# Optimization experiments

Measured on AMD Instinct MI355X. Metric: run time of the kernel, lower is better.

Reference implementation:

```python
import jax, jax.numpy as jnp
import numpy as np

N, E = 50000, 800000
H, C, K = 8, 16, 4
LAMBD = 1.0
DECAY = [float(np.log(LAMBD / (k + 1) + (1 + 1e-06))) for k in range(K + 1)]


def setup_inputs() -> dict:
    key = jax.random.key(0)
    ks = jax.random.split(key, 10)
    s = 0.05  # keep activations stable over K hops
    return {
        "x": jax.random.normal(ks[0], (N, 256), jnp.float32),
        "edge_index": jax.random.randint(ks[1], (2, E), 0, N, jnp.int64),
        "W0": jax.random.normal(ks[2], (256, 128), jnp.float32) * s,
        "b0": jnp.zeros((128,), jnp.float32),
        "W1": jax.random.normal(ks[3], (128, 128), jnp.float32) * s,
        "b1": jnp.zeros((128,), jnp.float32),
        "Wout": jax.random.normal(ks[4], (128, 40), jnp.float32) * s,
        "bout": jnp.zeros((40,), jnp.float32),
        "hop_att0": jax.random.normal(ks[5], (H, C), jnp.float32) * s,
        "hop_atts": jax.random.normal(ks[6], (K, H, 2 * C), jnp.float32) * s,
        "atts": jax.random.normal(ks[7], (K, H, C), jnp.float32) * s,
        "hop_biases": jnp.ones((K + 1, H), jnp.float32),
    }


def _aero_forward(x, edge_index, W0, b0, W1, b1, Wout, bout,
                  hop_att0, hop_atts, atts, hop_biases):
    n = x.shape[0]
    # add self loops (cached_edge_index is None in the torch module)
    loops = jnp.arange(n, dtype=edge_index.dtype)
    row = jnp.concatenate([edge_index[0], loops])  # source j
    col = jnp.concatenate([edge_index[1], loops])  # target i

    # hid_feat_init (dropout p=0 -> identity); num_layers=2
    h = x @ W0 + b0
    h = jax.nn.elu(h) @ W1 + b1
    h = h.reshape(n, H, C)

    # k = 0 hop attention
    g = jnp.einsum('hc,nhc->nh', hop_att0, jax.nn.elu(h)) + hop_biases[0]
    z = h * g[..., None]
    z_scale = z * DECAY[0]

    for k in range(1, K + 1):
        # edge attention: gather, elementwise, degree-normalize
        zi = z_scale[col]          # [E', H, C] target
        zj = z_scale[row]          # [E', H, C] source
        a = jnp.einsum('hc,ehc->eh', atts[k - 1], jax.nn.elu(zi + zj))
        a = jax.nn.softplus(a) + 1e-06                       # [E', H]
        deg = jax.ops.segment_sum(a, col, num_segments=n)    # [N, H]
        dinv = jnp.where(deg > 0, deg ** -0.5, 0.0)
        a = dinv[row] * a * dinv[col]
        # propagate: scatter-add weighted source features onto targets
        h = jax.ops.segment_sum(a[..., None] * h[row], col, num_segments=n)
        # hop attention on concat(h, z_scale)
        hz = jax.nn.elu(jnp.concatenate([h, z_scale], axis=-1))  # [N, H, 2C]
        g = jnp.einsum('hc,nhc->nh', hop_atts[k - 1], hz) + hop_biases[k]
        z = z + h * g[..., None]
        z_scale = z * DECAY[k]

    # node classifier
    z = jax.nn.elu(z.reshape(n, H * C))
    return z @ Wout + bout


def reference(x, edge_index, W0, b0, W1, b1, Wout, bout,
              hop_att0, hop_atts, atts, hop_biases):
    return _aero_forward(x, edge_index, W0, b0, W1, b1, Wout, bout,
                         hop_att0, hop_atts, atts, hop_biases)
```

## Files before the change

### kernel.cpp

```cpp
#include <hip/hip_runtime.h>
#include <hip/hip_fp16.h>
#include <math.h>

#define NH 8
#define NC 16
#define HC 128

typedef __attribute__((ext_vector_type(4))) _Float16 half4;
typedef __attribute__((ext_vector_type(8))) _Float16 half8;

__device__ __forceinline__ float eluf(float x) { return x > 0.f ? x : __expf(x) - 1.f; }
__device__ __forceinline__ float splusf(float x) { return fmaxf(x, 0.f) + __logf(1.f + __expf(-fabsf(x))); }

#if __has_builtin(__builtin_amdgcn_exp2f)
#define EXP2F(x) __builtin_amdgcn_exp2f(x)
#else
#define EXP2F(x) exp2f(x)
#endif

__global__ void count_kernel(const int* __restrict__ ei, int* __restrict__ cnt, int E, int E2) {
    int e = blockIdx.x * blockDim.x + threadIdx.x;
    if (e >= E2) return;
    int col = (e < E) ? ei[E + e] : (e - E);
    atomicAdd(&cnt[col], 1);
}

__global__ void scan1_kernel(const int* __restrict__ counts, int* __restrict__ ptr,
                             int* __restrict__ partials, int n) {
    __shared__ int tmp[256];
    int t = threadIdx.x;
    int i = blockIdx.x * 256 + t;
    int v = (i < n) ? counts[i] : 0;
    tmp[t] = v;
    __syncthreads();
    for (int off = 1; off < 256; off <<= 1) {
        int add = (t >= off) ? tmp[t - off] : 0;
        __syncthreads();
        tmp[t] += add;
        __syncthreads();
    }
    if (i < n) ptr[i] = tmp[t] - v;
    if (t == 255) partials[blockIdx.x] = tmp[255];
}

__global__ void scan2_kernel(int* __restrict__ partials, int nb) {
    __shared__ int tmp[256];
    int t = threadIdx.x;
    int v = (t < nb) ? partials[t] : 0;
    tmp[t] = v;
    __syncthreads();
    for (int off = 1; off < 256; off <<= 1) {
        int add = (t >= off) ? tmp[t - off] : 0;
        __syncthreads();
        tmp[t] += add;
        __syncthreads();
    }
    if (t < nb) partials[t] = tmp[t] - v;
}

__global__ void scan3_kernel(int* __restrict__ ptr, const int* __restrict__ partials,
                             int n, int total) {
    int i = blockIdx.x * 256 + threadIdx.x;
    if (i < n) ptr[i] += partials[blockIdx.x];
    if (i == 0) ptr[n] = total;
}

__global__ void fill_kernel(const int* __restrict__ ei, const int* __restrict__ ptr,
                            int* __restrict__ cursor, int* __restrict__ src, int E, int E2) {
    int e = blockIdx.x * blockDim.x + threadIdx.x;
    if (e >= E2) return;
    int col, row;
    if (e < E) { row = ei[e]; col = ei[E + e]; }
    else       { row = e - E; col = e - E; }
    int pos = ptr[col] + atomicAdd(&cursor[col], 1);
    src[pos] = row;
}

template<int K, bool ELU_OUT, bool HOP0>
__global__ __launch_bounds__(256)
void mlp_gemm(const float* __restrict__ A, const float* __restrict__ W,
              const float* __restrict__ bias, float* __restrict__ out, int M,
              float* __restrict__ z_out, _Float16* __restrict__ h16_out,
              _Float16* __restrict__ z16_out,
              const float* __restrict__ att0, const float* __restrict__ hb0) {
    __shared__ float As[16 * 68];
    __shared__ float Ws[16 * 132];
    const int tid = threadIdx.x;
    const int m0 = blockIdx.x * 64;
    const int tm = tid >> 4;
    const int tn = tid & 15;
    float acc[4][8];
#pragma unroll
    for (int i = 0; i < 4; ++i)
#pragma unroll
        for (int j = 0; j < 8; ++j) acc[i][j] = 0.f;

    const int ra = tid >> 2;
    const int qa = (tid & 3) * 4;

    for (int k0 = 0; k0 < K; k0 += 16) {
        float4 a = make_float4(0.f, 0.f, 0.f, 0.f);
        int garow = m0 + ra;
        if (garow < M) a = *(const float4*)(A + (size_t)garow * K + k0 + qa);
        float wv[8];
#pragma unroll
        for (int t = 0; t < 8; ++t) {
            int idx = tid + t * 256;
            int r = idx >> 7, c = idx & 127;
            wv[t] = W[(size_t)(k0 + r) * 128 + c];
        }
        __syncthreads();
        As[(qa + 0) * 68 + ra] = a.x; As[(qa + 1) * 68 + ra] = a.y;
        As[(qa + 2) * 68 + ra] = a.z; As[(qa + 3) * 68 + ra] = a.w;
#pragma unroll
        for (int t = 0; t < 8; ++t) {
            int idx = tid + t * 256;
            int r = idx >> 7, c = idx & 127;
            Ws[r * 132 + c] = wv[t];
        }
        __syncthreads();
#pragma unroll
        for (int kk = 0; kk < 16; ++kk) {
            float ar[4], wr[8];
            *(float4*)&ar[0] = *(const float4*)&As[kk * 68 + tm * 4];
            *(float4*)&wr[0] = *(const float4*)&Ws[kk * 132 + tn * 4];
            *(float4*)&wr[4] = *(const float4*)&Ws[kk * 132 + 64 + tn * 4];
#pragma unroll
            for (int i = 0; i < 4; ++i)
#pragma unroll
                for (int j = 0; j < 8; ++j)
                    acc[i][j] = fmaf(ar[i], wr[j], acc[i][j]);
        }
    }
#pragma unroll
    for (int i = 0; i < 4; ++i) {
        int r = m0 + tm * 4 + i;
        float vv[8];
#pragma unroll
        for (int c = 0; c < 2; ++c)
#pragma unroll
            for (int j = 0; j < 4; ++j) {
                float v = acc[i][c * 4 + j] + bias[c * 64 + tn * 4 + j];
                if (ELU_OUT) v = eluf(v);
                vv[c * 4 + j] = v;
            }
        if (HOP0) {
            float part[2];
#pragma unroll
            for (int c = 0; c < 2; ++c) {
                float p = 0.f;
#pragma unroll
                for (int j = 0; j < 4; ++j)
                    p += att0[c * 64 + tn * 4 + j] * eluf(vv[c * 4 + j]);
                p += __shfl_xor(p, 1);
                p += __shfl_xor(p, 2);
                part[c] = p;
            }
            if (r < M) {
#pragma unroll
                for (int c = 0; c < 2; ++c) {
                    float g = part[c] + hb0[4 * c + (tn >> 2)];
                    int coff = c * 64 + tn * 4;
                    _Float16* hp  = h16_out + ((size_t)r << 7) + coff;
                    _Float16* zhp = z16_out + ((size_t)r << 7) + coff;
                    float*    zp  = z_out   + ((size_t)r << 7) + coff;
                    half4 ho, zo;
                    float zz[4];
#pragma unroll
                    for (int j = 0; j < 4; ++j) zz[j] = vv[c * 4 + j] * g;
                    ho.x = (_Float16)vv[c * 4 + 0]; ho.y = (_Float16)vv[c * 4 + 1];
                    ho.z = (_Float16)vv[c * 4 + 2]; ho.w = (_Float16)vv[c * 4 + 3];
                    zo.x = (_Float16)zz[0]; zo.y = (_Float16)zz[1];
                    zo.z = (_Float16)zz[2]; zo.w = (_Float16)zz[3];
                    *(half4*)hp = ho;
                    *(half4*)zhp = zo;
                    *(float4*)zp = make_float4(zz[0], zz[1], zz[2], zz[3]);
                }
            }
        } else {
            if (r < M) {
#pragma unroll
                for (int c = 0; c < 2; ++c) {
                    float* op = out + (size_t)r * 128 + c * 64 + tn * 4;
                    *(float4*)op = make_float4(vv[c * 4 + 0], vv[c * 4 + 1],
                                               vv[c * 4 + 2], vv[c * 4 + 3]);
                }
            }
        }
    }
}

__global__ __launch_bounds__(256)
void passA_kernel(const _Float16* __restrict__ z16, const int* __restrict__ ptr,
                  const int* __restrict__ src, const float* __restrict__ att,
                  float decay, _Float16* __restrict__ a_e, float* __restrict__ dinv, int n) {
    int wid = (int)((blockIdx.x * 256u + threadIdx.x) >> 6);
    if (wid >= n) return;
    const int lane = threadIdx.x & 63;
    const int g  = lane >> 4;
    const int q  = lane & 15;
    const int hd = q >> 1;
    const unsigned i = (unsigned)wid;
    const float dl2 = decay * 1.44269504089f;

    float ziL[8];
    {
        const half8 zi = *(const half8*)(z16 + ((size_t)i << 7) + (q << 3));
#pragma unroll
        for (int c = 0; c < 8; ++c) ziL[c] = (float)zi[c] * dl2;
    }
    float av[8];
    *(float4*)&av[0] = *(const float4*)(att + (q << 3));
    *(float4*)&av[4] = *(const float4*)(att + (q << 3) + 4);
    float sav = ((av[0] + av[1]) + (av[2] + av[3]))
              + ((av[4] + av[5]) + (av[6] + av[7]));
    sav += __shfl_xor(sav, 1);

    const int s0 = ptr[wid], s1 = ptr[wid + 1];
    float dacc = 0.f;

#define PA_BODY(f, sv) do {                                                  \
        float pm = 0.f, pe = 0.f;                                            \
        _Pragma("unroll")                                                    \
        for (int c = 0; c < 8; ++c) {                                        \
            float y = fmaf((float)(f)[c], dl2, ziL[c]);                      \
            float e2 = EXP2F(fminf(y, 0.f));                                 \
            pm = fmaf(av[c], fmaxf(y, 0.f), pm);                             \
            pe = fmaf(av[c], e2, pe);                                        \
        }                                                                    \
        float pc = fmaf(pm, 0.69314718056f, pe);                             \
        pc += __shfl_xor(pc, 1);                                             \
        if ((q & 1) == 0) {                                                  \
            float aval = splusf(pc - sav) + 1e-6f;                           \
            a_e[((size_t)(sv) << 3) + hd] = (_Float16)aval;                  \
            dacc += aval;                                                    \
        }                                                                    \
    } while (0)

    const int nfull = (s1 - s0) & ~7;
    const int send = s0 + nfull;
    for (int s = s0 + g; s < send; s += 8) {
        unsigned ja = (unsigned)src[s];
        unsigned jb = (unsigned)src[s + 4];
        const half8 fa = *(const half8*)(z16 + ((size_t)ja << 7) + (q << 3));
        const half8 fb = *(const half8*)(z16 + ((size_t)jb << 7) + (q << 3));
        PA_BODY(fa, s);
        PA_BODY(fb, s + 4);
    }
    {
        int sA = send + g;
        if (sA < s1) {
            unsigned ja = (unsigned)src[sA];
            const half8 fa = *(const half8*)(z16 + ((size_t)ja << 7) + (q << 3));
            PA_BODY(fa, sA);
        }
        int sB = send + 4 + g;
        if (sB < s1) {
            unsigned jb = (unsigned)src[sB];
            const half8 fb = *(const half8*)(z16 + ((size_t)jb << 7) + (q << 3));
            PA_BODY(fb, sB);
        }
    }
#undef PA_BODY

    dacc += __shfl_xor(dacc, 16);
    dacc += __shfl_xor(dacc, 32);
    if ((lane & 0x31) == 0) {
        dinv[((size_t)i << 3) + hd] = (dacc > 0.f) ? (1.f / sqrtf(dacc)) : 0.f;
    }
}

__global__ __launch_bounds__(256)
void passB_kernel(const _Float16* __restrict__ h_in, float* __restrict__ z,
                  _Float16* __restrict__ z16,
                  const int* __restrict__ ptr, const int* __restrict__ src,
                  const _Float16* __restrict__ a_e, const float* __restrict__ dinv,
                  const float* __restrict__ hatt, const float* __restrict__ hb,
                  float decay, _Float16* __restrict__ h_out, int n, int store_h) {
    int wid = (int)((blockIdx.x * 256u + threadIdx.x) >> 6);
    if (wid >= n) return;
    const int lane = threadIdx.x & 63;
    const int g  = lane >> 4;
    const int q  = lane & 15;
    const int hd = q >> 1;
    const unsigned i = (unsigned)wid;

    const float di = dinv[((size_t)i << 3) + hd];
    const int s0 = ptr[wid], s1 = ptr[wid + 1];
    float acc[8];
#pragma unroll
    for (int c = 0; c < 8; ++c) acc[c] = 0.f;

    const int nfull = (s1 - s0) & ~7;
    const int send = s0 + nfull;
    for (int s = s0 + g; s < send; s += 8) {
        unsigned ja = (unsigned)src[s];
        unsigned jb = (unsigned)src[s + 4];
        const _Float16 aA = a_e[((size_t)s << 3) + hd];
        const _Float16 aB = a_e[((size_t)(s + 4) << 3) + hd];
        const float dA = dinv[((size_t)ja << 3) + hd];
        const float dB = dinv[((size_t)jb << 3) + hd];
        const half8 fa = *(const half8*)(h_in + ((size_t)ja << 7) + (q << 3));
        const half8 fb = *(const half8*)(h_in + ((size_t)jb << 7) + (q << 3));
        const float wa = (float)aA * dA;
        const float wb = (float)aB * dB;
#pragma unroll
        for (int c = 0; c < 8; ++c) acc[c] = fmaf((float)fa[c], wa, acc[c]);
#pragma unroll
        for (int c = 0; c < 8; ++c) acc[c] = fmaf((float)fb[c], wb, acc[c]);
    }
    {
        int sA = send + g;
        if (sA < s1) {
            unsigned j = (unsigned)src[sA];
            const float w = (float)a_e[((size_t)sA << 3) + hd] * dinv[((size_t)j << 3) + hd];
            const half8 f = *(const half8*)(h_in + ((size_t)j << 7) + (q << 3));
#pragma unroll
            for (int c = 0; c < 8; ++c) acc[c] = fmaf((float)f[c], w, acc[c]);
        }
        int sB = send + 4 + g;
        if (sB < s1) {
            unsigned j = (unsigned)src[sB];
            const float w = (float)a_e[((size_t)sB << 3) + hd] * dinv[((size_t)j << 3) + hd];
            const half8 f = *(const half8*)(h_in + ((size_t)j << 7) + (q << 3));
#pragma unroll
            for (int c = 0; c < 8; ++c) acc[c] = fmaf((float)f[c], w, acc[c]);
        }
    }
#pragma unroll
    for (int c = 0; c < 8; ++c) {
        acc[c] += __shfl_xor(acc[c], 16);
        acc[c] += __shfl_xor(acc[c], 32);
    }

    float hn[8];
#pragma unroll
    for (int c = 0; c < 8; ++c) hn[c] = di * acc[c];

    float* zrow = z + ((size_t)i << 7) + (q << 3);
    const float4 zva = *(const float4*)zrow;
    const float4 zvb = *(const float4*)(zrow + 4);
    float zv[8] = {zva.x, zva.y, zva.z, zva.w, zvb.x, zvb.y, zvb.z, zvb.w};

    const float* hA = hatt + hd * 32 + (q & 1) * 8;
    float p = 0.f;
#pragma unroll
    for (int c = 0; c < 8; ++c) p = fmaf(hA[c], eluf(hn[c]), p);
#pragma unroll
    for (int c = 0; c < 8; ++c) p = fmaf(hA[16 + c], eluf(zv[c] * decay), p);
    p += __shfl_xor(p, 1);
    const float gv = p + hb[hd];

    if (g == 0) {
        float zn[8];
#pragma unroll
        for (int c = 0; c < 8; ++c) zn[c] = fmaf(hn[c], gv, zv[c]);
        *(float4*)zrow       = make_float4(zn[0], zn[1], zn[2], zn[3]);
        *(float4*)(zrow + 4) = make_float4(zn[4], zn[5], zn[6], zn[7]);
        if (store_h) {
            half8 ho, zo;
#pragma unroll
            for (int c = 0; c < 8; ++c) { ho[c] = (_Float16)hn[c]; zo[c] = (_Float16)zn[c]; }
            *(half8*)(h_out + ((size_t)i << 7) + (q << 3)) = ho;
            *(half8*)(z16   + ((size_t)i << 7) + (q << 3)) = zo;
        }
    }
}

__global__ __launch_bounds__(256)
void gout_kernel(const float* __restrict__ z, const float* __restrict__ W,
                 const float* __restrict__ bias, float* __restrict__ out, int M) {
    __shared__ float zs[128 * 65];
    __shared__ float ws[128 * 40];
    const int tid = threadIdx.x;
    const int r0 = blockIdx.x * 64;
    for (int idx = tid; idx < 128 * 40; idx += 256) ws[idx] = W[idx];
    const int r = tid >> 2;
    const int q = tid & 3;
    {
        int grow = r0 + r;
#pragma unroll
        for (int t = 0; t < 8; ++t) {
            int k = q * 4 + t * 16;
            float4 v = make_float4(0.f, 0.f, 0.f, 0.f);
            if (grow < M) v = *(const float4*)(z + (size_t)grow * HC + k);
            zs[(k + 0) * 65 + r] = eluf(v.x);
            zs[(k + 1) * 65 + r] = eluf(v.y);
            zs[(k + 2) * 65 + r] = eluf(v.z);
            zs[(k + 3) * 65 + r] = eluf(v.w);
        }
    }
    __syncthreads();
    float acc[10];
#pragma unroll
    for (int j = 0; j < 10; ++j) acc[j] = bias[q * 10 + j];
    for (int k = 0; k < 128; ++k) {
        float zk = zs[k * 65 + r];
#pragma unroll
        for (int j = 0; j < 10; ++j)
            acc[j] = fmaf(zk, ws[k * 40 + q * 10 + j], acc[j]);
    }
    int grow = r0 + r;
    if (grow < M) {
        float* op = out + (size_t)grow * 40 + q * 10;
#pragma unroll
        for (int j = 0; j < 10; ++j) op[j] = acc[j];
    }
}

extern "C" void kernel_launch(void* const* d_in, const int* in_sizes, int n_in,
                              void* d_out, int out_size, void* d_ws, size_t ws_size,
                              hipStream_t stream) {
    (void)n_in; (void)out_size; (void)ws_size;
    const float* x    = (const float*)d_in[0];
    const int*   ei   = (const int*)d_in[1];
    const float* W0   = (const float*)d_in[2];
    const float* b0   = (const float*)d_in[3];
    const float* W1   = (const float*)d_in[4];
    const float* b1   = (const float*)d_in[5];
    const float* Wout = (const float*)d_in[6];
    const float* bout = (const float*)d_in[7];
    const float* att0 = (const float*)d_in[8];
    const float* hatts= (const float*)d_in[9];
    const float* atts = (const float*)d_in[10];
    const float* hb   = (const float*)d_in[11];
    float* out = (float*)d_out;

    const int N  = in_sizes[0] / 256;
    const int E  = in_sizes[1] / 2;
    const int E2 = E + N;

    char* p = (char*)d_ws;
    auto carve = [&](size_t bytes) -> char* {
        char* r = p;
        p += (bytes + 255) & ~(size_t)255;
        return r;
    };
    float*    h1     = (float*)carve((size_t)N * HC * 4);
    _Float16* hbufA  = (_Float16*)carve((size_t)N * HC * 2);
    _Float16* hbufB  = (_Float16*)carve((size_t)N * HC * 2);
    float*    zbuf   = (float*)carve((size_t)N * HC * 4);
    _Float16* z16buf = (_Float16*)carve((size_t)N * HC * 2);
    _Float16* a_e    = (_Float16*)carve((size_t)E2 * NH * 2);
    float*    dinvb  = (float*)carve((size_t)N * NH * 4);
    int* csr_ptr   = (int*)carve((size_t)(N + 1) * 4);
    int* csr_src   = (int*)carve((size_t)E2 * 4);
    int* cursor    = (int*)carve((size_t)N * 4);
    int* partials  = (int*)carve(1024 * 4);

    float decay[5];
    for (int k = 0; k <= 4; ++k) decay[k] = (float)log(1.0 / (k + 1) + 1.0 + 1e-6);

    hipMemsetAsync(cursor, 0, (size_t)N * 4, stream);
    int eb = (E2 + 255) / 256;
    int nb = (N + 255) / 256;
    count_kernel<<<eb, 256, 0, stream>>>(ei, cursor, E, E2);
    scan1_kernel<<<nb, 256, 0, stream>>>(cursor, csr_ptr, partials, N);
    scan2_kernel<<<1, 256, 0, stream>>>(partials, nb);
    scan3_kernel<<<nb, 256, 0, stream>>>(csr_ptr, partials, N, E2);
    hipMemsetAsync(cursor, 0, (size_t)N * 4, stream);
    fill_kernel<<<eb, 256, 0, stream>>>(ei, csr_ptr, cursor, csr_src, E, E2);

    int gb = (N + 63) / 64;
    mlp_gemm<256, true , false><<<gb, 256, 0, stream>>>(x,  W0, b0, h1, N,
                                                        nullptr, nullptr, nullptr,
                                                        nullptr, nullptr);
    mlp_gemm<128, false, true ><<<gb, 256, 0, stream>>>(h1, W1, b1, nullptr, N,
                                                        zbuf, hbufA, z16buf, att0, hb);

    _Float16* hin  = hbufA;
    _Float16* hout = hbufB;
    int wb = (N + 3) / 4;
    for (int k = 1; k <= 4; ++k) {
        passA_kernel<<<wb, 256, 0, stream>>>(z16buf, csr_ptr, csr_src,
                                             atts + (size_t)(k - 1) * NH * NC,
                                             decay[k - 1], a_e, dinvb, N);
        passB_kernel<<<wb, 256, 0, stream>>>(hin, zbuf, z16buf, csr_ptr, csr_src,
                                             a_e, dinvb,
                                             hatts + (size_t)(k - 1) * NH * 32,
                                             hb + (size_t)k * NH, decay[k - 1], hout, N,
                                             (k < 4) ? 1 : 0);
        _Float16* t = hin; hin = hout; hout = t;
    }

    gout_kernel<<<(N + 63) / 64, 256, 0, stream>>>(zbuf, Wout, bout, out, N);
}
```

Measured before the change: 671.9 us.

## Replace FP32 SIMT MLP GEMMs with FP16 MFMA and pre-swizzled weights

The two dense MLP layers move from an FP32 shared-memory SIMT GEMM to the 16x16x32 f16 MFMA instruction. Weights are converted and swizzled into per-lane fragment order by a small prep kernel. The intermediate activation is stored as FP16 in a padded buffer, which halves its traffic. The epilogue goes through shared memory so each wave handles whole heads, which changes how the hop-0 attention reduction is done. The cost is reduced input precision (x and W rounded to fp16) and two extra tiny launches.

```diff
diff --git a/kernel.cpp b/kernel.cpp
--- a/kernel.cpp
+++ b/kernel.cpp
@@ -6,8 +6,8 @@
 #define NC 16
 #define HC 128
 
-typedef __attribute__((ext_vector_type(4))) _Float16 half4;
 typedef __attribute__((ext_vector_type(8))) _Float16 half8;
+typedef __attribute__((ext_vector_type(4))) float f32x4;
 
 __device__ __forceinline__ float eluf(float x) { return x > 0.f ? x : __expf(x) - 1.f; }
 __device__ __forceinline__ float splusf(float x) { return fmaxf(x, 0.f) + __logf(1.f + __expf(-fabsf(x))); }
@@ -76,116 +76,153 @@
     src[pos] = row;
 }
 
-template<int K, bool ELU_OUT, bool HOP0>
+__global__ void wswz_kernel(const float* __restrict__ W, _Float16* __restrict__ Wf, int NKS) {
+    int t = blockIdx.x * 256 + threadIdx.x;
+    if (t >= 8 * NKS * 64) return;
+    int lane = t & 63;
+    int ks = (t >> 6) % NKS;
+    int cg = (t >> 6) / NKS;
+    int n = cg * 16 + (lane & 15);
+    int k0 = ks * 32 + (lane >> 4) * 8;
+    half8 v;
+#pragma unroll
+    for (int j = 0; j < 8; ++j) v[j] = (_Float16)W[(size_t)(k0 + j) * 128 + n];
+    *(half8*)(Wf + (size_t)t * 8) = v;
+}
+
+template<int K, bool A16, bool HOP0>
 __global__ __launch_bounds__(256)
-void mlp_gemm(const float* __restrict__ A, const float* __restrict__ W,
-              const float* __restrict__ bias, float* __restrict__ out, int M,
-              float* __restrict__ z_out, _Float16* __restrict__ h16_out,
-              _Float16* __restrict__ z16_out,
-              const float* __restrict__ att0, const float* __restrict__ hb0) {
-    __shared__ float As[16 * 68];
-    __shared__ float Ws[16 * 132];
+void mfma_gemm(const float* __restrict__ A32, const _Float16* __restrict__ A16p,
+               const _Float16* __restrict__ Wf, const float* __restrict__ bias,
+               int M, _Float16* __restrict__ h1_out,
+               float* __restrict__ z_out, _Float16* __restrict__ h16_out,
+               _Float16* __restrict__ z16_out,
+               const float* __restrict__ att0, const float* __restrict__ hb0) {
+    constexpr int NKS = K / 32;
+    __shared__ float sL[64 * 132];
     const int tid = threadIdx.x;
+    const int w = tid >> 6;
+    const int lane = tid & 63;
+    const int l15 = lane & 15;
+    const int lg = lane >> 4;
     const int m0 = blockIdx.x * 64;
-    const int tm = tid >> 4;
-    const int tn = tid & 15;
-    float acc[4][8];
-#pragma unroll
-    for (int i = 0; i < 4; ++i)
-#pragma unroll
-        for (int j = 0; j < 8; ++j) acc[i][j] = 0.f;
-
-    const int ra = tid >> 2;
-    const int qa = (tid & 3) * 4;
-
-    for (int k0 = 0; k0 < K; k0 += 16) {
-        float4 a = make_float4(0.f, 0.f, 0.f, 0.f);
-        int garow = m0 + ra;
-        if (garow < M) a = *(const float4*)(A + (size_t)garow * K + k0 + qa);
-        float wv[8];
-#pragma unroll
-        for (int t = 0; t < 8; ++t) {
-            int idx = tid + t * 256;
-            int r = idx >> 7, c = idx & 127;
-            wv[t] = W[(size_t)(k0 + r) * 128 + c];
-        }
-        __syncthreads();
-        As[(qa + 0) * 68 + ra] = a.x; As[(qa + 1) * 68 + ra] = a.y;
-        As[(qa + 2) * 68 + ra] = a.z; As[(qa + 3) * 68 + ra] = a.w;
-#pragma unroll
-        for (int t = 0; t < 8; ++t) {
-            int idx = tid + t * 256;
-            int r = idx >> 7, c = idx & 127;
-            Ws[r * 132 + c] = wv[t];
-        }
-        __syncthreads();
-#pragma unroll
-        for (int kk = 0; kk < 16; ++kk) {
-            float ar[4], wr[8];
-            *(float4*)&ar[0] = *(const float4*)&As[kk * 68 + tm * 4];
-            *(float4*)&wr[0] = *(const float4*)&Ws[kk * 132 + tn * 4];
-            *(float4*)&wr[4] = *(const float4*)&Ws[kk * 132 + 64 + tn * 4];
-#pragma unroll
-            for (int i = 0; i < 4; ++i)
-#pragma unroll
-                for (int j = 0; j < 8; ++j)
-                    acc[i][j] = fmaf(ar[i], wr[j], acc[i][j]);
-        }
-    }
-#pragma unroll
-    for (int i = 0; i < 4; ++i) {
-        int r = m0 + tm * 4 + i;
-        float vv[8];
-#pragma unroll
-        for (int c = 0; c < 2; ++c)
-#pragma unroll
-            for (int j = 0; j < 4; ++j) {
-                float v = acc[i][c * 4 + j] + bias[c * 64 + tn * 4 + j];
-                if (ELU_OUT) v = eluf(v);
-                vv[c * 4 + j] = v;
-            }
-        if (HOP0) {
-            float part[2];
-#pragma unroll
-            for (int c = 0; c < 2; ++c) {
-                float p = 0.f;
-#pragma unroll
-                for (int j = 0; j < 4; ++j)
-                    p += att0[c * 64 + tn * 4 + j] * eluf(vv[c * 4 + j]);
-                p += __shfl_xor(p, 1);
-                p += __shfl_xor(p, 2);
-                part[c] = p;
-            }
-            if (r < M) {
-#pragma unroll
-                for (int c = 0; c < 2; ++c) {
-                    float g = part[c] + hb0[4 * c + (tn >> 2)];
-                    int coff = c * 64 + tn * 4;
-                    _Float16* hp  = h16_out + ((size_t)r << 7) + coff;
-                    _Float16* zhp = z16_out + ((size_t)r << 7) + coff;
-                    float*    zp  = z_out   + ((size_t)r << 7) + coff;
-                    half4 ho, zo;
-                    float zz[4];
-#pragma unroll
-                    for (int j = 0; j < 4; ++j) zz[j] = vv[c * 4 + j] * g;
-                    ho.x = (_Float16)vv[c * 4 + 0]; ho.y = (_Float16)vv[c * 4 + 1];
-                    ho.z = (_Float16)vv[c * 4 + 2]; ho.w = (_Float16)vv[c * 4 + 3];
-                    zo.x = (_Float16)zz[0]; zo.y = (_Float16)zz[1];
-                    zo.z = (_Float16)zz[2]; zo.w = (_Float16)zz[3];
-                    *(half4*)hp = ho;
-                    *(half4*)zhp = zo;
-                    *(float4*)zp = make_float4(zz[0], zz[1], zz[2], zz[3]);
-                }
+
+    f32x4 acc[4][2];
+#pragma unroll
+    for (int a = 0; a < 4; ++a)
+#pragma unroll
+        for (int b = 0; b < 2; ++b)
+            acc[a][b] = f32x4{0.f, 0.f, 0.f, 0.f};
+
+#pragma unroll
+    for (int ks = 0; ks < NKS; ++ks) {
+        const int kb = ks * 32 + lg * 8;
+        half8 af[4];
+        if (A16) {
+#pragma unroll
+            for (int mf = 0; mf < 4; ++mf) {
+                int row = m0 + mf * 16 + l15;
+                af[mf] = *(const half8*)(A16p + ((size_t)row << 7) + kb);
             }
         } else {
-            if (r < M) {
-#pragma unroll
-                for (int c = 0; c < 2; ++c) {
-                    float* op = out + (size_t)r * 128 + c * 64 + tn * 4;
-                    *(float4*)op = make_float4(vv[c * 4 + 0], vv[c * 4 + 1],
-                                               vv[c * 4 + 2], vv[c * 4 + 3]);
+#pragma unroll
+            for (int mf = 0; mf < 4; ++mf) {
+                int row = m0 + mf * 16 + l15;
+                float4 a0 = make_float4(0.f, 0.f, 0.f, 0.f), a1 = a0;
+                if (row < M) {
+                    const float* ap = A32 + (size_t)row * K + kb;
+                    a0 = *(const float4*)ap;
+                    a1 = *(const float4*)(ap + 4);
                 }
+                half8 h;
+                h[0] = (_Float16)a0.x; h[1] = (_Float16)a0.y;
+                h[2] = (_Float16)a0.z; h[3] = (_Float16)a0.w;
+                h[4] = (_Float16)a1.x; h[5] = (_Float16)a1.y;
+                h[6] = (_Float16)a1.z; h[7] = (_Float16)a1.w;
+                af[mf] = h;
             }
+        }
+        half8 bf[2];
+#pragma unroll
+        for (int cf = 0; cf < 2; ++cf) {
+            int cg = w * 2 + cf;
+            bf[cf] = *(const half8*)(Wf + (size_t)((cg * NKS + ks) * 64 + lane) * 8);
+        }
+#pragma unroll
+        for (int mf = 0; mf < 4; ++mf)
+#pragma unroll
+            for (int cf = 0; cf < 2; ++cf)
+                acc[mf][cf] = __builtin_amdgcn_mfma_f32_16x16x32_f16(af[mf], bf[cf],
+                                                                     acc[mf][cf], 0, 0, 0);
+    }
+
+#pragma unroll
+    for (int mf = 0; mf < 4; ++mf)
+#pragma unroll
+        for (int cf = 0; cf < 2; ++cf) {
+            int col = w * 32 + cf * 16 + l15;
+#pragma unroll
+            for (int r = 0; r < 4; ++r)
+                sL[(mf * 16 + lg * 4 + r) * 132 + col] = acc[mf][cf][r];
+        }
+    __syncthreads();
+
+    const int rr = lane;
+    const int q = w;
+    const int row = m0 + rr;
+    float v[32];
+#pragma unroll
+    for (int t = 0; t < 8; ++t)
+        *(float4*)&v[t * 4] = *(const float4*)&sL[rr * 132 + q * 32 + t * 4];
+#pragma unroll
+    for (int t = 0; t < 8; ++t) {
+        float4 bv = *(const float4*)&bias[q * 32 + t * 4];
+        v[t * 4 + 0] += bv.x; v[t * 4 + 1] += bv.y;
+        v[t * 4 + 2] += bv.z; v[t * 4 + 3] += bv.w;
+    }
+
+    if (!HOP0) {
+        if (row < M) {
+            half8 o[4];
+#pragma unroll
+            for (int c = 0; c < 32; ++c) o[c >> 3][c & 7] = (_Float16)eluf(v[c]);
+            _Float16* hp = h1_out + ((size_t)row << 7) + q * 32;
+#pragma unroll
+            for (int t = 0; t < 4; ++t) *(half8*)(hp + t * 8) = o[t];
+        }
+    } else {
+        float g[2];
+#pragma unroll
+        for (int hh = 0; hh < 2; ++hh) {
+            int head = q * 2 + hh;
+            float p = 0.f;
+#pragma unroll
+            for (int c = 0; c < 16; ++c)
+                p = fmaf(att0[head * 16 + c], eluf(v[hh * 16 + c]), p);
+            g[hh] = p + hb0[head];
+        }
+        if (row < M) {
+            float zz[32];
+#pragma unroll
+            for (int c = 0; c < 32; ++c) zz[c] = v[c] * g[c >> 4];
+            half8 ho[4], zo[4];
+#pragma unroll
+            for (int c = 0; c < 32; ++c) {
+                ho[c >> 3][c & 7] = (_Float16)v[c];
+                zo[c >> 3][c & 7] = (_Float16)zz[c];
+            }
+            _Float16* hp  = h16_out + ((size_t)row << 7) + q * 32;
+            _Float16* zhp = z16_out + ((size_t)row << 7) + q * 32;
+            float*    zp  = z_out   + ((size_t)row << 7) + q * 32;
+#pragma unroll
+            for (int t = 0; t < 4; ++t) {
+                *(half8*)(hp + t * 8) = ho[t];
+                *(half8*)(zhp + t * 8) = zo[t];
+            }
+#pragma unroll
+            for (int t = 0; t < 8; ++t)
+                *(float4*)(zp + t * 4) = make_float4(zz[t * 4 + 0], zz[t * 4 + 1],
+                                                     zz[t * 4 + 2], zz[t * 4 + 3]);
         }
     }
 }
@@ -429,6 +466,7 @@
     const int N  = in_sizes[0] / 256;
     const int E  = in_sizes[1] / 2;
     const int E2 = E + N;
+    const size_t Npad = ((size_t)N + 63) & ~(size_t)63;
 
     char* p = (char*)d_ws;
     auto carve = [&](size_t bytes) -> char* {
@@ -436,13 +474,15 @@
         p += (bytes + 255) & ~(size_t)255;
         return r;
     };
-    float*    h1     = (float*)carve((size_t)N * HC * 4);
+    _Float16* h1     = (_Float16*)carve(Npad * HC * 2);
     _Float16* hbufA  = (_Float16*)carve((size_t)N * HC * 2);
     _Float16* hbufB  = (_Float16*)carve((size_t)N * HC * 2);
     float*    zbuf   = (float*)carve((size_t)N * HC * 4);
     _Float16* z16buf = (_Float16*)carve((size_t)N * HC * 2);
     _Float16* a_e    = (_Float16*)carve((size_t)E2 * NH * 2);
     float*    dinvb  = (float*)carve((size_t)N * NH * 4);
+    _Float16* Wf0    = (_Float16*)carve((size_t)8 * 8 * 64 * 8 * 2);
+    _Float16* Wf1    = (_Float16*)carve((size_t)8 * 4 * 64 * 8 * 2);
     int* csr_ptr   = (int*)carve((size_t)(N + 1) * 4);
     int* csr_src   = (int*)carve((size_t)E2 * 4);
     int* cursor    = (int*)carve((size_t)N * 4);
@@ -461,12 +501,14 @@
     hipMemsetAsync(cursor, 0, (size_t)N * 4, stream);
     fill_kernel<<<eb, 256, 0, stream>>>(ei, csr_ptr, cursor, csr_src, E, E2);
 
+    wswz_kernel<<<16, 256, 0, stream>>>(W0, Wf0, 8);
+    wswz_kernel<<<8, 256, 0, stream>>>(W1, Wf1, 4);
+
     int gb = (N + 63) / 64;
-    mlp_gemm<256, true , false><<<gb, 256, 0, stream>>>(x,  W0, b0, h1, N,
-                                                        nullptr, nullptr, nullptr,
-                                                        nullptr, nullptr);
-    mlp_gemm<128, false, true ><<<gb, 256, 0, stream>>>(h1, W1, b1, nullptr, N,
-                                                        zbuf, hbufA, z16buf, att0, hb);
+    mfma_gemm<256, false, false><<<gb, 256, 0, stream>>>(
+        x, nullptr, Wf0, b0, N, h1, nullptr, nullptr, nullptr, nullptr, nullptr);
+    mfma_gemm<128, true, true><<<gb, 256, 0, stream>>>(
+        nullptr, h1, Wf1, b1, N, nullptr, zbuf, hbufA, z16buf, att0, hb);
 
     _Float16* hin  = hbufA;
     _Float16* hout = hbufB;
```

New measurement: 670.7 us. About the same (-0.2%).
